# Kernel optimization log

Hardware: AMD Instinct MI355X
Metric: run time of the kernel (lower is better)

The kernel has to match this reference:

```python
import jax, jax.numpy as jnp
import numpy as np

THRESHOLD = 0.0025
EPS = 1e-12
NORM_EPS = 1e-12  # torch F.normalize default eps


def _l2n(x):
    # F.normalize(x, p=2, dim=1): x / max(||x||_2, eps)
    n = jnp.sqrt(jnp.sum(x * x, axis=1, keepdims=True))
    return x / jnp.maximum(n, NORM_EPS)


def _memory_unit(feature, memory):
    # feature: [N, C], memory: [M, C]
    nf = _l2n(feature)
    nm = _l2n(memory)
    w = jax.nn.softmax(nf @ nm.T, axis=1)            # [N, M] cosine sims -> softmax
    # hard_shrink: relu(w - t) * w / (|w - t| + eps)
    w = jax.nn.relu(w - THRESHOLD) * w / (jnp.abs(w - THRESHOLD) + EPS)
    # L1 normalize rows
    w = w / jnp.maximum(jnp.sum(jnp.abs(w), axis=1, keepdims=True), NORM_EPS)
    mf = w @ memory                                   # [N, C] memory read
    return mf, w


def setup_inputs() -> dict:
    key = jax.random.key(0)
    ks = jax.random.split(key, 6)
    N, M = 16384, 1024
    chans = [256, 512, 1024]
    d = {}
    for i, c in enumerate(chans):
        d[f"feat{i}"] = jax.random.normal(ks[i], (N, c), dtype=jnp.float32)
        d[f"mem{i}"] = jax.random.normal(ks[3 + i], (M, c), dtype=jnp.float32)
    return d


def reference(feat0, feat1, feat2, mem0, mem1, mem2):
    outs = []
    weights = []
    for f, m in ((feat0, mem0), (feat1, mem1), (feat2, mem2)):
        mf, w = _memory_unit(f, m)
        outs.append(jnp.concatenate((mf, f), axis=1))  # cat along channel dim
        weights.append(w)
    return (outs[0], outs[1], outs[2], weights[0], weights[1], weights[2])
```

## Files before the change

kernel.cpp:

```cpp
#include <hip/hip_runtime.h>
#include <stdint.h>

typedef float f32x4 __attribute__((ext_vector_type(4)));
typedef short s16x8 __attribute__((ext_vector_type(8)));
typedef short s16x4 __attribute__((ext_vector_type(4)));

static constexpr int NR = 16384;

__device__ __forceinline__ unsigned short f2bf(float f) {
    uint32_t u = __float_as_uint(f);
    u += 0x7FFFu + ((u >> 16) & 1u);
    return (unsigned short)(u >> 16);
}

template<int C>
__device__ __forceinline__ void prep_body(const float* __restrict__ mp,
                                          short* __restrict__ nmp,
                                          int ct, short* stage) {
    const int tid = threadIdx.x;
    const int row = tid >> 4;
    const int c4  = tid & 15;
    constexpr int IT = C / 64;
    const f32x4* src = (const f32x4*)(mp + (size_t)(ct * 16 + row) * C);
    f32x4 vals[IT];
    float ss = 0.f;
#pragma unroll
    for (int i = 0; i < IT; ++i) {
        f32x4 v = src[c4 + 16 * i];
        vals[i] = v;
        ss += v.x * v.x + v.y * v.y + v.z * v.z + v.w * v.w;
    }
#pragma unroll
    for (int m = 1; m < 16; m <<= 1) ss += __shfl_xor(ss, m);
    const float inv = 1.f / fmaxf(sqrtf(ss), 1e-12f);
#pragma unroll
    for (int i = 0; i < IT; ++i) {
        f32x4 v = vals[i];
        s16x4 o;
        o[0] = (short)f2bf(v.x * inv);
        o[1] = (short)f2bf(v.y * inv);
        o[2] = (short)f2bf(v.z * inv);
        o[3] = (short)f2bf(v.w * inv);
        *(s16x4*)&stage[row * C + (c4 + 16 * i) * 4] = o;
    }
    __syncthreads();
    const int lane = tid & 63;
    const int wv = tid >> 6;
    constexpr int NKB = C / 32;
#pragma unroll
    for (int j = 0; j < NKB / 4; ++j) {
        const int kb = j * 4 + wv;
        const s16x8 v = *(const s16x8*)&stage[(lane & 15) * C + kb * 32 + (lane >> 4) * 8];
        *(s16x8*)&nmp[((size_t)ct * NKB + kb) * 512 + lane * 8] = v;
    }
}

__global__ __launch_bounds__(256) void prep_all(const float* m0, short* n0,
                                                const float* m1, short* n1,
                                                const float* m2, short* n2) {
    __shared__ short stage[16 * 1024];
    const int bid = blockIdx.x;
    if (bid < 64) prep_body<256>(m0, n0, bid, stage);
    else if (bid < 128) prep_body<512>(m1, n1, bid - 64, stage);
    else prep_body<1024>(m2, n2, bid - 128, stage);
}

template<int C>
__device__ __forceinline__ void copy_body(const float* __restrict__ feat,
                                          float* __restrict__ out_cat,
                                          float* __restrict__ inv_arr, int tt) {
    const int tid = threadIdx.x;
    const int row = tid >> 4;
    const int c4  = tid & 15;
    constexpr int IT = C / 64;
    const f32x4* src = (const f32x4*)(feat + (size_t)(tt * 16 + row) * C);
    f32x4* dstf = (f32x4*)(out_cat + (size_t)(tt * 16 + row) * (2 * C) + C);
    f32x4* dstz = (f32x4*)(out_cat + (size_t)(tt * 16 + row) * (2 * C));
    const f32x4 z4 = {0.f, 0.f, 0.f, 0.f};
    float ss = 0.f;
#pragma unroll
    for (int i = 0; i < IT; ++i) {
        const int idx = c4 + 16 * i;
        f32x4 v = __builtin_nontemporal_load(&src[idx]);
        __builtin_nontemporal_store(v, &dstf[idx]);
        __builtin_nontemporal_store(z4, &dstz[idx]);
        ss += v.x * v.x + v.y * v.y + v.z * v.z + v.w * v.w;
    }
#pragma unroll
    for (int m = 1; m < 16; m <<= 1) ss += __shfl_xor(ss, m);
    if (c4 == 0) inv_arr[tt * 16 + row] = 1.f / fmaxf(sqrtf(ss), 1e-12f);
}

__global__ __launch_bounds__(256) void copy_all(const float* f0, float* o0,
                                                const float* f1, float* o1,
                                                const float* f2, float* o2,
                                                float* invA) {
    const int bid = blockIdx.x;
    if (bid < 1024) copy_body<1024>(f2, o2, invA + 2 * NR, bid);
    else if (bid < 2048) copy_body<512>(f1, o1, invA + NR, bid - 1024);
    else copy_body<256>(f0, o0, invA, bid - 2048);
}

template<int C>
__device__ __forceinline__ void gemm_body(const float* __restrict__ feat,
                                          const float* __restrict__ memv,
                                          const short* __restrict__ nm,
                                          const float* __restrict__ inv_arr,
                                          float* __restrict__ out_cat,
                                          float* __restrict__ out_w,
                                          int tile,
                                          short* __restrict__ As,
                                          float (*__restrict__ red)[64],
                                          float* __restrict__ rowT,
                                          float* __restrict__ rowL,
                                          float* __restrict__ invL,
                                          int* __restrict__ rowflag,
                                          int* __restrict__ anyflag) {
    constexpr int NKB = C / 32;
    constexpr int NCH = C / 64;
    const int tid  = threadIdx.x;
    const int w    = tid >> 6;
    const int lane = tid & 63;
    const int g    = lane >> 4;
    const int ml   = lane & 15;
    const int swz  = ml & 7;
    const int row0 = tile * 64;

    const int frow = tid >> 4;
    const int fk4  = tid & 15;
    const float* fsrc = feat + (size_t)(row0 + frow) * C + fk4 * 4;
    const int ldsW = frow * 64 + (((fk4 >> 1) ^ (frow & 7)) << 3) + (fk4 & 1) * 4;
    const short* nbB = nm + (size_t)(w * 4) * NKB * 512 + lane * 8;

    if (tid == 0) *anyflag = 0;
    if (tid < 64) invL[tid] = inv_arr[row0 + tid];

    f32x4 acc[4][4];
#pragma unroll
    for (int r = 0; r < 4; ++r)
#pragma unroll
        for (int ct = 0; ct < 4; ++ct)
            acc[r][ct] = (f32x4){0.f, 0.f, 0.f, 0.f};

    {
        const f32x4 v = *(const f32x4*)fsrc;
        s16x4 o;
        o[0] = (short)f2bf(v.x); o[1] = (short)f2bf(v.y);
        o[2] = (short)f2bf(v.z); o[3] = (short)f2bf(v.w);
        *(s16x4*)&As[ldsW] = o;
    }
    f32x4 fnxt;
    if (NCH > 1) fnxt = *(const f32x4*)(fsrc + 64);
    s16x8 bc[4];
#pragma unroll
    for (int ct = 0; ct < 4; ++ct)
        bc[ct] = *(const s16x8*)(nbB + (size_t)ct * NKB * 512);
    asm volatile("s_waitcnt lgkmcnt(0)" ::: "memory");
    __builtin_amdgcn_s_barrier();
    asm volatile("" ::: "memory");

    for (int kb = 0; kb < NKB; ++kb) {
        const int chunk = kb >> 1;
        if ((kb & 1) == 0 && chunk + 1 < NCH) {
            s16x4 o;
            o[0] = (short)f2bf(fnxt.x); o[1] = (short)f2bf(fnxt.y);
            o[2] = (short)f2bf(fnxt.z); o[3] = (short)f2bf(fnxt.w);
            *(s16x4*)&As[((chunk + 1) & 1) * 4096 + ldsW] = o;
            if (chunk + 2 < NCH)
                fnxt = *(const f32x4*)(fsrc + (size_t)(chunk + 2) * 64);
        }
        s16x8 bn[4];
        const bool more = (kb + 1 < NKB);
        if (more) {
#pragma unroll
            for (int ct = 0; ct < 4; ++ct)
                bn[ct] = *(const s16x8*)(nbB + ((size_t)ct * NKB + kb + 1) * 512);
        }
        const short* Ab = &As[(chunk & 1) * 4096];
        const int gr = ((kb & 1) << 2) | g;
        s16x8 a[4];
#pragma unroll
        for (int r = 0; r < 4; ++r)
            a[r] = *(const s16x8*)&Ab[(r * 16 + ml) * 64 + ((gr ^ swz) << 3)];
        __builtin_amdgcn_s_setprio(1);
#pragma unroll
        for (int r = 0; r < 4; ++r)
#pragma unroll
            for (int ct = 0; ct < 4; ++ct)
                acc[r][ct] = __builtin_amdgcn_mfma_f32_16x16x32_bf16(a[r], bc[ct], acc[r][ct], 0, 0, 0);
        __builtin_amdgcn_s_setprio(0);
        if (more) {
#pragma unroll
            for (int ct = 0; ct < 4; ++ct) bc[ct] = bn[ct];
        }
        if ((kb & 1) == 1 && kb + 1 < NKB) {
            asm volatile("s_waitcnt lgkmcnt(0)" ::: "memory");
            __builtin_amdgcn_s_barrier();
            asm volatile("" ::: "memory");
        }
    }
    __syncthreads();

    float IL[4][4];

#pragma unroll
    for (int r = 0; r < 4; ++r)
#pragma unroll
        for (int i = 0; i < 4; ++i) {
            const float inv = invL[r * 16 + 4 * g + i];
            float s = 0.f;
#pragma unroll
            for (int ct = 0; ct < 4; ++ct) {
                const float e = __expf(acc[r][ct][i] * inv);
                acc[r][ct][i] = e;
                s += e;
            }
#pragma unroll
            for (int m = 1; m < 16; m <<= 1) s += __shfl_xor(s, m);
            if (ml == 0) red[w][r * 16 + 4 * g + i] = s;
        }
    __syncthreads();
    if (tid < 64) {
        float t = red[0][tid];
#pragma unroll
        for (int ww = 1; ww < 16; ++ww) t += red[ww][tid];
        rowT[tid] = 1.f / t;
    }
    __syncthreads();

#pragma unroll
    for (int r = 0; r < 4; ++r)
#pragma unroll
        for (int i = 0; i < 4; ++i) {
            const float tinv = rowT[r * 16 + 4 * g + i];
            float l1 = 0.f;
#pragma unroll
            for (int ct = 0; ct < 4; ++ct) {
                const float wv = acc[r][ct][i] * tinv;
                const float d = wv - 0.0025f;
                const float v = (d > 0.f) ? (d * wv / (d + 1e-12f)) : 0.f;
                acc[r][ct][i] = v;
                l1 += v;
            }
#pragma unroll
            for (int m = 1; m < 16; m <<= 1) l1 += __shfl_xor(l1, m);
            if (ml == 0) red[w][r * 16 + 4 * g + i] = l1;
        }
    __syncthreads();
    if (tid < 64) {
        float t = red[0][tid];
#pragma unroll
        for (int ww = 1; ww < 16; ++ww) t += red[ww][tid];
        rowL[tid] = 1.f / fmaxf(t, 1e-12f);
        rowflag[tid] = (t > 0.f) ? 1 : 0;
        if (t > 0.f) *anyflag = 1;
    }
    __syncthreads();

#pragma unroll
    for (int r = 0; r < 4; ++r)
#pragma unroll
        for (int i = 0; i < 4; ++i) {
            const float il = rowL[r * 16 + 4 * g + i];
            float* orow = out_w + (size_t)(row0 + r * 16 + 4 * g + i) * 1024;
#pragma unroll
            for (int ct = 0; ct < 4; ++ct)
                orow[(w * 4 + ct) * 16 + ml] = acc[r][ct][i] * il;
        }
    __threadfence_block();
    __syncthreads();

    if (*anyflag != 0) {
        constexpr int CC = C / 64;
#pragma unroll
        for (int rr = 0; rr < 4; ++rr) {
            const int row = w * 4 + rr;
            if (!rowflag[row]) continue;
            float* dst = out_cat + (size_t)(row0 + row) * (2 * C);
            float mfacc[CC];
#pragma unroll
            for (int cc = 0; cc < CC; ++cc) mfacc[cc] = 0.f;
            const float* wrow = out_w + (size_t)(row0 + row) * 1024;
            for (int jb = 0; jb < 1024; jb += 64) {
                const float wv = wrow[jb + lane];
                unsigned long long msk = __ballot(wv != 0.f);
                while (msk) {
                    const int j = __builtin_ctzll(msk);
                    msk &= msk - 1;
                    const float val = __shfl(wv, j);
                    const float* mrow = memv + (size_t)(jb + j) * C;
#pragma unroll
                    for (int cc = 0; cc < CC; ++cc)
                        mfacc[cc] += val * mrow[cc * 64 + lane];
                }
            }
#pragma unroll
            for (int cc = 0; cc < CC; ++cc) dst[cc * 64 + lane] = mfacc[cc];
        }
    }
}

__global__ __launch_bounds__(1024) void gemm_all(
        const float* f0, const float* m0, const short* n0, float* o0, float* w0,
        const float* f1, const float* m1, const short* n1, float* o1, float* w1,
        const float* f2, const float* m2, const short* n2, float* o2, float* w2,
        const float* invA) {
    __shared__ short As[2 * 4096];
    __shared__ float red[16][64];
    __shared__ float rowT[64];
    __shared__ float rowL[64];
    __shared__ float invL[64];
    __shared__ int rowflag[64];
    __shared__ int anyflag;

    const int bid = blockIdx.x;
    if (bid < 256)
        gemm_body<1024>(f2, m2, n2, invA + 2 * NR, o2, w2, bid,
                        As, red, rowT, rowL, invL, rowflag, &anyflag);
    else if (bid < 512)
        gemm_body<512>(f1, m1, n1, invA + NR, o1, w1, bid - 256,
                       As, red, rowT, rowL, invL, rowflag, &anyflag);
    else
        gemm_body<256>(f0, m0, n0, invA, o0, w0, bid - 512,
                       As, red, rowT, rowL, invL, rowflag, &anyflag);
}

extern "C" void kernel_launch(void* const* d_in, const int* in_sizes, int n_in,
                              void* d_out, int out_size, void* d_ws, size_t ws_size,
                              hipStream_t stream) {
    const float* feat[3] = {nullptr, nullptr, nullptr};
    const float* memp[3] = {nullptr, nullptr, nullptr};
    for (int i = 0; i < n_in && i < 6; ++i) {
        const int s = in_sizes[i];
        const float* p = (const float*)d_in[i];
        if (s == 16384 * 256) feat[0] = p;
        else if (s == 16384 * 512) feat[1] = p;
        else if (s == 16384 * 1024) feat[2] = p;
        else if (s == 1024 * 256) memp[0] = p;
        else if (s == 1024 * 512) memp[1] = p;
        else if (s == 1024 * 1024) memp[2] = p;
    }
    float* out = (float*)d_out;
    short* nm0 = (short*)d_ws;
    short* nm1 = nm0 + 1024 * 256;
    short* nm2 = nm1 + 1024 * 512;
    float* invA = (float*)(nm2 + 1024 * 1024);

    const size_t O0 = 0;
    const size_t O1 = (size_t)16384 * 512;
    const size_t O2 = O1 + (size_t)16384 * 1024;
    const size_t W0 = O2 + (size_t)16384 * 2048;
    const size_t W1 = W0 + (size_t)16384 * 1024;
    const size_t W2 = W1 + (size_t)16384 * 1024;

    prep_all<<<192, 256, 0, stream>>>(memp[0], nm0, memp[1], nm1, memp[2], nm2);

    copy_all<<<3072, 256, 0, stream>>>(feat[0], out + O0,
                                       feat[1], out + O1,
                                       feat[2], out + O2, invA);

    gemm_all<<<768, 1024, 0, stream>>>(
        feat[0], memp[0], nm0, out + O0, out + W0,
        feat[1], memp[1], nm1, out + O1, out + W1,
        feat[2], memp[2], nm2, out + O2, out + W2, invA);
}
```

Measured before the change: 200.1 us.

## Stream B tiles into LDS via async global_load_lds and fuse row norms into GEMM

The per-wave register double-buffered B fragment loads become asynchronous global-to-LDS loads into a 128KB double-buffered LDS stage, guarded by vmcnt waits, so the memory fetch overlaps the MFMA work. The feature row L2 norm is now accumulated inside the GEMM from the already-loaded feature values, which removes that reduction and the inverse-norm array from the copy kernel. The large LDS allocation limits blocks per CU, and the inline vmcnt counting has to stay in step with the other outstanding global loads.

```diff
diff --git a/kernel.cpp b/kernel.cpp
--- a/kernel.cpp
+++ b/kernel.cpp
@@ -11,6 +11,12 @@
     uint32_t u = __float_as_uint(f);
     u += 0x7FFFu + ((u >> 16) & 1u);
     return (unsigned short)(u >> 16);
+}
+
+__device__ __forceinline__ void g2l16(const short* g, short* l) {
+    __builtin_amdgcn_global_load_lds(
+        (const __attribute__((address_space(1))) uint32_t*)g,
+        (__attribute__((address_space(3))) uint32_t*)l, 16, 0, 0);
 }
 
 template<int C>
@@ -67,8 +73,7 @@
 
 template<int C>
 __device__ __forceinline__ void copy_body(const float* __restrict__ feat,
-                                          float* __restrict__ out_cat,
-                                          float* __restrict__ inv_arr, int tt) {
+                                          float* __restrict__ out_cat, int tt) {
     const int tid = threadIdx.x;
     const int row = tid >> 4;
     const int c4  = tid & 15;
@@ -77,38 +82,32 @@
     f32x4* dstf = (f32x4*)(out_cat + (size_t)(tt * 16 + row) * (2 * C) + C);
     f32x4* dstz = (f32x4*)(out_cat + (size_t)(tt * 16 + row) * (2 * C));
     const f32x4 z4 = {0.f, 0.f, 0.f, 0.f};
-    float ss = 0.f;
 #pragma unroll
     for (int i = 0; i < IT; ++i) {
         const int idx = c4 + 16 * i;
         f32x4 v = __builtin_nontemporal_load(&src[idx]);
         __builtin_nontemporal_store(v, &dstf[idx]);
         __builtin_nontemporal_store(z4, &dstz[idx]);
-        ss += v.x * v.x + v.y * v.y + v.z * v.z + v.w * v.w;
-    }
-#pragma unroll
-    for (int m = 1; m < 16; m <<= 1) ss += __shfl_xor(ss, m);
-    if (c4 == 0) inv_arr[tt * 16 + row] = 1.f / fmaxf(sqrtf(ss), 1e-12f);
+    }
 }
 
 __global__ __launch_bounds__(256) void copy_all(const float* f0, float* o0,
                                                 const float* f1, float* o1,
-                                                const float* f2, float* o2,
-                                                float* invA) {
+                                                const float* f2, float* o2) {
     const int bid = blockIdx.x;
-    if (bid < 1024) copy_body<1024>(f2, o2, invA + 2 * NR, bid);
-    else if (bid < 2048) copy_body<512>(f1, o1, invA + NR, bid - 1024);
-    else copy_body<256>(f0, o0, invA, bid - 2048);
+    if (bid < 1024) copy_body<1024>(f2, o2, bid);
+    else if (bid < 2048) copy_body<512>(f1, o1, bid - 1024);
+    else copy_body<256>(f0, o0, bid - 2048);
 }
 
 template<int C>
 __device__ __forceinline__ void gemm_body(const float* __restrict__ feat,
                                           const float* __restrict__ memv,
                                           const short* __restrict__ nm,
-                                          const float* __restrict__ inv_arr,
                                           float* __restrict__ out_cat,
                                           float* __restrict__ out_w,
                                           int tile,
+                                          short* __restrict__ Bst,
                                           short* __restrict__ As,
                                           float (*__restrict__ red)[64],
                                           float* __restrict__ rowT,
@@ -130,10 +129,11 @@
     const int fk4  = tid & 15;
     const float* fsrc = feat + (size_t)(row0 + frow) * C + fk4 * 4;
     const int ldsW = frow * 64 + (((fk4 >> 1) ^ (frow & 7)) << 3) + (fk4 & 1) * 4;
-    const short* nbB = nm + (size_t)(w * 4) * NKB * 512 + lane * 8;
+    const short* nbG = nm + (size_t)(w * 4) * NKB * 512 + lane * 8;
+    short* bD0 = Bst + (w * 4) * 512 + lane * 8;
+    short* bD1 = Bst + 32768 + (w * 4) * 512 + lane * 8;
 
     if (tid == 0) *anyflag = 0;
-    if (tid < 64) invL[tid] = inv_arr[row0 + tid];
 
     f32x4 acc[4][4];
 #pragma unroll
@@ -142,8 +142,17 @@
         for (int ct = 0; ct < 4; ++ct)
             acc[r][ct] = (f32x4){0.f, 0.f, 0.f, 0.f};
 
+    float ss = 0.f;
+
+#pragma unroll
+    for (int p = 0; p < 4; ++p)
+        g2l16(nbG + (size_t)p * NKB * 512, bD0 + p * 512 - lane * 8 + lane * 8);
+#pragma unroll
+    for (int p = 0; p < 4; ++p)
+        g2l16(nbG + ((size_t)p * NKB + 1) * 512, bD1 + p * 512);
     {
         const f32x4 v = *(const f32x4*)fsrc;
+        ss += v.x * v.x + v.y * v.y + v.z * v.z + v.w * v.w;
         s16x4 o;
         o[0] = (short)f2bf(v.x); o[1] = (short)f2bf(v.y);
         o[2] = (short)f2bf(v.z); o[3] = (short)f2bf(v.w);
@@ -151,10 +160,6 @@
     }
     f32x4 fnxt;
     if (NCH > 1) fnxt = *(const f32x4*)(fsrc + 64);
-    s16x8 bc[4];
-#pragma unroll
-    for (int ct = 0; ct < 4; ++ct)
-        bc[ct] = *(const s16x8*)(nbB + (size_t)ct * NKB * 512);
     asm volatile("s_waitcnt lgkmcnt(0)" ::: "memory");
     __builtin_amdgcn_s_barrier();
     asm volatile("" ::: "memory");
@@ -162,6 +167,7 @@
     for (int kb = 0; kb < NKB; ++kb) {
         const int chunk = kb >> 1;
         if ((kb & 1) == 0 && chunk + 1 < NCH) {
+            ss += fnxt.x * fnxt.x + fnxt.y * fnxt.y + fnxt.z * fnxt.z + fnxt.w * fnxt.w;
             s16x4 o;
             o[0] = (short)f2bf(fnxt.x); o[1] = (short)f2bf(fnxt.y);
             o[2] = (short)f2bf(fnxt.z); o[3] = (short)f2bf(fnxt.w);
@@ -169,39 +175,45 @@
             if (chunk + 2 < NCH)
                 fnxt = *(const f32x4*)(fsrc + (size_t)(chunk + 2) * 64);
         }
-        s16x8 bn[4];
-        const bool more = (kb + 1 < NKB);
-        if (more) {
-#pragma unroll
-            for (int ct = 0; ct < 4; ++ct)
-                bn[ct] = *(const s16x8*)(nbB + ((size_t)ct * NKB + kb + 1) * 512);
-        }
+        if (kb < NKB - 1) asm volatile("s_waitcnt vmcnt(4)" ::: "memory");
+        else              asm volatile("s_waitcnt vmcnt(0)" ::: "memory");
+        const short* Bb = Bst + (kb & 1) * 32768 + (w * 4) * 512 + lane * 8;
+        s16x8 b[4];
+#pragma unroll
+        for (int p = 0; p < 4; ++p)
+            b[p] = *(const s16x8*)(Bb + p * 512);
         const short* Ab = &As[(chunk & 1) * 4096];
         const int gr = ((kb & 1) << 2) | g;
         s16x8 a[4];
 #pragma unroll
         for (int r = 0; r < 4; ++r)
             a[r] = *(const s16x8*)&Ab[(r * 16 + ml) * 64 + ((gr ^ swz) << 3)];
+        asm volatile("s_waitcnt lgkmcnt(0)" ::: "memory");
+        __builtin_amdgcn_sched_barrier(0);
+        if (kb + 2 < NKB) {
+            short* bDn = Bst + (kb & 1) * 32768 + (w * 4) * 512 + lane * 8;
+#pragma unroll
+            for (int p = 0; p < 4; ++p)
+                g2l16(nbG + ((size_t)p * NKB + kb + 2) * 512, bDn + p * 512);
+        }
         __builtin_amdgcn_s_setprio(1);
 #pragma unroll
         for (int r = 0; r < 4; ++r)
 #pragma unroll
             for (int ct = 0; ct < 4; ++ct)
-                acc[r][ct] = __builtin_amdgcn_mfma_f32_16x16x32_bf16(a[r], bc[ct], acc[r][ct], 0, 0, 0);
+                acc[r][ct] = __builtin_amdgcn_mfma_f32_16x16x32_bf16(a[r], b[ct], acc[r][ct], 0, 0, 0);
         __builtin_amdgcn_s_setprio(0);
-        if (more) {
-#pragma unroll
-            for (int ct = 0; ct < 4; ++ct) bc[ct] = bn[ct];
-        }
         if ((kb & 1) == 1 && kb + 1 < NKB) {
             asm volatile("s_waitcnt lgkmcnt(0)" ::: "memory");
             __builtin_amdgcn_s_barrier();
             asm volatile("" ::: "memory");
         }
     }
-    __syncthreads();
-
-    float IL[4][4];
+
+#pragma unroll
+    for (int m = 1; m < 16; m <<= 1) ss += __shfl_xor(ss, m);
+    if (fk4 == 0) invL[frow] = 1.f / fmaxf(sqrtf(ss), 1e-12f);
+    __syncthreads();
 
 #pragma unroll
     for (int r = 0; r < 4; ++r)
@@ -303,8 +315,8 @@
 __global__ __launch_bounds__(1024) void gemm_all(
         const float* f0, const float* m0, const short* n0, float* o0, float* w0,
         const float* f1, const float* m1, const short* n1, float* o1, float* w1,
-        const float* f2, const float* m2, const short* n2, float* o2, float* w2,
-        const float* invA) {
+        const float* f2, const float* m2, const short* n2, float* o2, float* w2) {
+    __shared__ short Bst[2 * 32768];
     __shared__ short As[2 * 4096];
     __shared__ float red[16][64];
     __shared__ float rowT[64];
@@ -315,14 +327,14 @@
 
     const int bid = blockIdx.x;
     if (bid < 256)
-        gemm_body<1024>(f2, m2, n2, invA + 2 * NR, o2, w2, bid,
-                        As, red, rowT, rowL, invL, rowflag, &anyflag);
+        gemm_body<1024>(f2, m2, n2, o2, w2, bid,
+                        Bst, As, red, rowT, rowL, invL, rowflag, &anyflag);
     else if (bid < 512)
-        gemm_body<512>(f1, m1, n1, invA + NR, o1, w1, bid - 256,
-                       As, red, rowT, rowL, invL, rowflag, &anyflag);
+        gemm_body<512>(f1, m1, n1, o1, w1, bid - 256,
+                       Bst, As, red, rowT, rowL, invL, rowflag, &anyflag);
     else
-        gemm_body<256>(f0, m0, n0, invA, o0, w0, bid - 512,
-                       As, red, rowT, rowL, invL, rowflag, &anyflag);
+        gemm_body<256>(f0, m0, n0, o0, w0, bid - 512,
+                       Bst, As, red, rowT, rowL, invL, rowflag, &anyflag);
 }
 
 extern "C" void kernel_launch(void* const* d_in, const int* in_sizes, int n_in,
@@ -344,7 +356,6 @@
     short* nm0 = (short*)d_ws;
     short* nm1 = nm0 + 1024 * 256;
     short* nm2 = nm1 + 1024 * 512;
-    float* invA = (float*)(nm2 + 1024 * 1024);
 
     const size_t O0 = 0;
     const size_t O1 = (size_t)16384 * 512;
@@ -357,10 +368,10 @@
 
     copy_all<<<3072, 256, 0, stream>>>(feat[0], out + O0,
                                        feat[1], out + O1,
-                                       feat[2], out + O2, invA);
+                                       feat[2], out + O2);
 
     gemm_all<<<768, 1024, 0, stream>>>(
         feat[0], memp[0], nm0, out + O0, out + W0,
         feat[1], memp[1], nm1, out + O1, out + W1,
-        feat[2], memp[2], nm2, out + O2, out + W2, invA);
-}
+        feat[2], memp[2], nm2, out + O2, out + W2);
+}
```

After: 187.1 us. -6.5%, faster.
